# Kernel tuning notes

Hardware: AMD Instinct MI355X
Metric: run time of the kernel (lower is better)

## Reference

```python
import jax, jax.numpy as jnp
import numpy as np

SM_SCALE = 0.08838834764831845  # 1/sqrt(128)
SLIDING_WINDOW = 128
N_TOKENS, N_HEADS, Q_MULT, D_HEAD = 2048, 8, 4, 128


def setup_inputs() -> dict:
    key = jax.random.key(0)
    k1, k2, k3, k4 = jax.random.split(key, 4)
    Q = jax.random.normal(k1, (N_TOKENS, N_HEADS, Q_MULT, D_HEAD), dtype=jnp.float32)
    K = jax.random.normal(k2, (N_TOKENS, N_HEADS, D_HEAD), dtype=jnp.float32)
    V = jax.random.normal(k3, (N_TOKENS, N_HEADS, D_HEAD), dtype=jnp.float32)
    S = jax.random.normal(k4, (N_HEADS * Q_MULT,), dtype=jnp.float32)
    return {"Q": Q, "K": K, "V": V, "S": S}


def _build_mask(n_tokens, sliding_window, dtype):
    q_idx = jnp.arange(n_tokens)[:, None]
    k_idx = jnp.arange(n_tokens)[None, :]
    # causal: disallow k > q; sliding window: disallow k <= q - sliding_window
    disallowed = k_idx > q_idx
    if sliding_window > 0:
        disallowed = disallowed | (k_idx <= q_idx - sliding_window)
    return jnp.where(disallowed, jnp.array(-jnp.inf, dtype), jnp.array(0.0, dtype))


def reference(Q, K, V, S):
    n_tokens, n_heads, q_mult, d_head = Q.shape
    mask = _build_mask(n_tokens, SLIDING_WINDOW, Q.dtype)  # (T, T)
    # scores: (h, m, q, k)
    QK = jnp.einsum('qhmd,khd->hmqk', Q, K) * SM_SCALE
    QK = QK + mask[None, None, :, :]
    # append per-(head, q_mult) sink logit as an extra key column
    sink = jnp.broadcast_to(S.reshape(n_heads, q_mult, 1, 1),
                            (n_heads, q_mult, n_tokens, 1))
    QK = jnp.concatenate([QK, sink], axis=-1)  # (h, m, q, k+1)
    W = jax.nn.softmax(QK, axis=-1)[..., :-1]  # drop sink column
    attn = jnp.einsum('hmqk,khd->qhmd', W, V)
    return attn.reshape(n_tokens, n_heads * q_mult * d_head)
```

## Files before the change

kernel.cpp:

```cpp
#include <hip/hip_runtime.h>
#include <cstdint>

#define T_TOK 2048
#define NH 8
#define QM 4
#define DH 128
#define BQ 32
#define ROWS 128
#define CK 32
#define KS 136
#define VS 40
#define PS 40
#define SM_SCALE 0.08838834764831845f

typedef __attribute__((ext_vector_type(8))) short short8v;
typedef __attribute__((ext_vector_type(4))) short short4v;
typedef __attribute__((ext_vector_type(4))) float floatx4;

static __device__ __forceinline__ short f2bf(float x) {
  union { float f; unsigned u; } v; v.f = x;
  return (short)((v.u + 0x7fffu + ((v.u >> 16) & 1u)) >> 16);
}

__global__ __launch_bounds__(512, 4)
void attn_fwd(const float* __restrict__ Qp, const float* __restrict__ Kp,
              const float* __restrict__ Vp, const float* __restrict__ Sp,
              float* __restrict__ Op) {
  __shared__ short k_s[2][CK * KS];
  __shared__ short v_s[2][DH * VS];
  __shared__ short p_s[ROWS * PS];

  const int t    = threadIdx.x;
  const int lane = t & 63;
  const int wv   = t >> 6;
  const int quad = lane >> 4;
  const int l16  = lane & 15;

  const int bx = blockIdx.x;
  const int h  = bx & 7;
  const int q0 = (bx >> 3) * BQ;
  const int lo0 = q0 > 127 ? q0 - 127 : 0;
  const int nk  = q0 + BQ - lo0;
  const int nch = (nk + CK - 1) >> 5;

  const int Ra = wv * 16 + l16;
  const int qa = q0 + (Ra >> 2), ma = Ra & 3;
  const float* qptr = Qp + ((size_t)qa * (NH * QM) + h * QM + ma) * DH + quad * 8;
  short8v qf[4];
#pragma unroll
  for (int s = 0; s < 4; ++s) {
    float4 x0 = *(const float4*)(qptr + 32 * s);
    float4 x1 = *(const float4*)(qptr + 32 * s + 4);
    short8v f;
    f[0] = f2bf(x0.x); f[1] = f2bf(x0.y); f[2] = f2bf(x0.z); f[3] = f2bf(x0.w);
    f[4] = f2bf(x1.x); f[5] = f2bf(x1.y); f[6] = f2bf(x1.z); f[7] = f2bf(x1.w);
    qf[s] = f;
  }

  const int kj  = t >> 5;
  const int kd4 = (t & 31) * 4;
  const int vd  = t & 127;
  const int vg  = t >> 7;

  const int qc = q0 + wv * 4 + quad;
  float dn[4] = {0.f, 0.f, 0.f, 0.f};
  floatx4 oacc[8];
#pragma unroll
  for (int nt = 0; nt < 8; ++nt) oacc[nt] = (floatx4)0.0f;

  float4 pk[2];
  float  pv[8];
  {
    const int kb = lo0;
#pragma unroll
    for (int p = 0; p < 2; ++p) {
      int g = kb + kj + 16 * p; g = g < T_TOK ? g : T_TOK - 1;
      pk[p] = *(const float4*)(Kp + ((size_t)g * NH + h) * DH + kd4);
    }
#pragma unroll
    for (int j = 0; j < 8; ++j) {
      int g = kb + vg * 8 + j; g = g < T_TOK ? g : T_TOK - 1;
      pv[j] = Vp[((size_t)g * NH + h) * DH + vd];
    }
  }

  for (int c = 0; c < nch; ++c) {
    const int b  = c & 1;
    const int kb = lo0 + c * CK;

#pragma unroll
    for (int p = 0; p < 2; ++p) {
      short4v s4;
      s4[0] = f2bf(pk[p].x); s4[1] = f2bf(pk[p].y);
      s4[2] = f2bf(pk[p].z); s4[3] = f2bf(pk[p].w);
      *(short4v*)(&k_s[b][(kj + 16 * p) * KS + kd4]) = s4;
    }
    {
      short8v s8;
#pragma unroll
      for (int j = 0; j < 8; ++j) s8[j] = f2bf(pv[j]);
      *(short8v*)(&v_s[b][vd * VS + vg * 8]) = s8;
    }
    __syncthreads();

    if (c + 1 < nch) {
      const int kb2 = kb + CK;
#pragma unroll
      for (int p = 0; p < 2; ++p) {
        int g = kb2 + kj + 16 * p; g = g < T_TOK ? g : T_TOK - 1;
        pk[p] = *(const float4*)(Kp + ((size_t)g * NH + h) * DH + kd4);
      }
#pragma unroll
      for (int j = 0; j < 8; ++j) {
        int g = kb2 + vg * 8 + j; g = g < T_TOK ? g : T_TOK - 1;
        pv[j] = Vp[((size_t)g * NH + h) * DH + vd];
      }
    }

    floatx4 sc0 = (floatx4)0.0f, sc1 = (floatx4)0.0f;
#pragma unroll
    for (int s = 0; s < 4; ++s) {
      short8v k0 = *(const short8v*)(&k_s[b][l16 * KS + quad * 8 + 32 * s]);
      short8v k1 = *(const short8v*)(&k_s[b][(l16 + 16) * KS + quad * 8 + 32 * s]);
      sc0 = __builtin_amdgcn_mfma_f32_16x16x32_bf16(qf[s], k0, sc0, 0, 0, 0);
      sc1 = __builtin_amdgcn_mfma_f32_16x16x32_bf16(qf[s], k1, sc1, 0, 0, 0);
    }

    const int k0i = kb + l16, k1i = kb + 16 + l16;
    const bool ok0 = (k0i <= qc) && (k0i > qc - 128);
    const bool ok1 = (k1i <= qc) && (k1i > qc - 128);
#pragma unroll
    for (int r = 0; r < 4; ++r) {
      float e0 = ok0 ? __expf(sc0[r] * SM_SCALE) : 0.f;
      float e1 = ok1 ? __expf(sc1[r] * SM_SCALE) : 0.f;
      dn[r] += e0 + e1;
      const int R = wv * 16 + quad * 4 + r;
      p_s[R * PS + l16]      = f2bf(e0);
      p_s[R * PS + 16 + l16] = f2bf(e1);
    }

    short8v pf = *(const short8v*)(&p_s[(wv * 16 + l16) * PS + quad * 8]);
#pragma unroll
    for (int nt = 0; nt < 8; ++nt) {
      short8v vf = *(const short8v*)(&v_s[b][(l16 + 16 * nt) * VS + quad * 8]);
      oacc[nt] = __builtin_amdgcn_mfma_f32_16x16x32_bf16(pf, vf, oacc[nt], 0, 0, 0);
    }
  }

#pragma unroll
  for (int r = 0; r < 4; ++r) {
    float s = dn[r];
#pragma unroll
    for (int mm = 1; mm <= 8; mm <<= 1) s += __shfl_xor(s, mm);
    const float total = s + __expf(Sp[h * QM + r]);
    const float rd = 1.0f / total;
    float* ob = Op + (size_t)qc * (NH * QM * DH) + ((size_t)h * QM + r) * DH + l16;
#pragma unroll
    for (int nt = 0; nt < 8; ++nt) ob[nt * 16] = oacc[nt][r] * rd;
  }
}

extern "C" void kernel_launch(void* const* d_in, const int* in_sizes, int n_in,
                              void* d_out, int out_size, void* d_ws, size_t ws_size,
                              hipStream_t stream) {
  const float* Q = (const float*)d_in[0];
  const float* K = (const float*)d_in[1];
  const float* V = (const float*)d_in[2];
  const float* S = (const float*)d_in[3];
  float* O = (float*)d_out;
  const int grid = (T_TOK / BQ) * NH;
  attn_fwd<<<dim3(grid), dim3(512), 0, stream>>>(Q, K, V, S, O);
}
```

Baseline: 104.4 us.

## Double query tile per block and interleave keys for vectorized P stores

```diff
diff --git a/kernel.cpp b/kernel.cpp
--- a/kernel.cpp
+++ b/kernel.cpp
@@ -5,8 +5,8 @@
 #define NH 8
 #define QM 4
 #define DH 128
-#define BQ 32
-#define ROWS 128
+#define BQ 64
+#define ROWS 256
 #define CK 32
 #define KS 136
 #define VS 40
@@ -15,6 +15,7 @@
 
 typedef __attribute__((ext_vector_type(8))) short short8v;
 typedef __attribute__((ext_vector_type(4))) short short4v;
+typedef __attribute__((ext_vector_type(2))) short short2v;
 typedef __attribute__((ext_vector_type(4))) float floatx4;
 
 static __device__ __forceinline__ short f2bf(float x) {
@@ -22,7 +23,7 @@
   return (short)((v.u + 0x7fffu + ((v.u >> 16) & 1u)) >> 16);
 }
 
-__global__ __launch_bounds__(512, 4)
+__global__ __launch_bounds__(1024, 4)
 void attn_fwd(const float* __restrict__ Qp, const float* __restrict__ Kp,
               const float* __restrict__ Vp, const float* __restrict__ Sp,
               float* __restrict__ Op) {
@@ -68,19 +69,17 @@
 #pragma unroll
   for (int nt = 0; nt < 8; ++nt) oacc[nt] = (floatx4)0.0f;
 
-  float4 pk[2];
-  float  pv[8];
+  float4 pk;
+  float  pv[4];
   {
-    const int kb = lo0;
+    int g = lo0 + kj; g = g < T_TOK ? g : T_TOK - 1;
+    pk = *(const float4*)(Kp + ((size_t)g * NH + h) * DH + kd4);
 #pragma unroll
-    for (int p = 0; p < 2; ++p) {
-      int g = kb + kj + 16 * p; g = g < T_TOK ? g : T_TOK - 1;
-      pk[p] = *(const float4*)(Kp + ((size_t)g * NH + h) * DH + kd4);
-    }
-#pragma unroll
-    for (int j = 0; j < 8; ++j) {
-      int g = kb + vg * 8 + j; g = g < T_TOK ? g : T_TOK - 1;
-      pv[j] = Vp[((size_t)g * NH + h) * DH + vd];
+    for (int u = 0; u < 4; ++u) {
+      const int s = vg * 4 + u;
+      int gk = lo0 + (s >> 1) + ((s & 1) << 4);
+      gk = gk < T_TOK ? gk : T_TOK - 1;
+      pv[u] = Vp[((size_t)gk * NH + h) * DH + vd];
     }
   }
 
@@ -88,32 +87,26 @@
     const int b  = c & 1;
     const int kb = lo0 + c * CK;
 
-#pragma unroll
-    for (int p = 0; p < 2; ++p) {
+    {
       short4v s4;
-      s4[0] = f2bf(pk[p].x); s4[1] = f2bf(pk[p].y);
-      s4[2] = f2bf(pk[p].z); s4[3] = f2bf(pk[p].w);
-      *(short4v*)(&k_s[b][(kj + 16 * p) * KS + kd4]) = s4;
-    }
-    {
-      short8v s8;
-#pragma unroll
-      for (int j = 0; j < 8; ++j) s8[j] = f2bf(pv[j]);
-      *(short8v*)(&v_s[b][vd * VS + vg * 8]) = s8;
+      s4[0] = f2bf(pk.x); s4[1] = f2bf(pk.y); s4[2] = f2bf(pk.z); s4[3] = f2bf(pk.w);
+      *(short4v*)(&k_s[b][kj * KS + kd4]) = s4;
+      short4v t4;
+      t4[0] = f2bf(pv[0]); t4[1] = f2bf(pv[1]); t4[2] = f2bf(pv[2]); t4[3] = f2bf(pv[3]);
+      *(short4v*)(&v_s[b][vd * VS + vg * 4]) = t4;
     }
     __syncthreads();
 
     if (c + 1 < nch) {
       const int kb2 = kb + CK;
+      int g = kb2 + kj; g = g < T_TOK ? g : T_TOK - 1;
+      pk = *(const float4*)(Kp + ((size_t)g * NH + h) * DH + kd4);
 #pragma unroll
-      for (int p = 0; p < 2; ++p) {
-        int g = kb2 + kj + 16 * p; g = g < T_TOK ? g : T_TOK - 1;
-        pk[p] = *(const float4*)(Kp + ((size_t)g * NH + h) * DH + kd4);
-      }
-#pragma unroll
-      for (int j = 0; j < 8; ++j) {
-        int g = kb2 + vg * 8 + j; g = g < T_TOK ? g : T_TOK - 1;
-        pv[j] = Vp[((size_t)g * NH + h) * DH + vd];
+      for (int u = 0; u < 4; ++u) {
+        const int s = vg * 4 + u;
+        int gk = kb2 + (s >> 1) + ((s & 1) << 4);
+        gk = gk < T_TOK ? gk : T_TOK - 1;
+        pv[u] = Vp[((size_t)gk * NH + h) * DH + vd];
       }
     }
 
@@ -135,8 +128,8 @@
       float e1 = ok1 ? __expf(sc1[r] * SM_SCALE) : 0.f;
       dn[r] += e0 + e1;
       const int R = wv * 16 + quad * 4 + r;
-      p_s[R * PS + l16]      = f2bf(e0);
-      p_s[R * PS + 16 + l16] = f2bf(e1);
+      short2v p2; p2[0] = f2bf(e0); p2[1] = f2bf(e1);
+      *(short2v*)(&p_s[R * PS + 2 * l16]) = p2;
     }
 
     short8v pf = *(const short8v*)(&p_s[(wv * 16 + l16) * PS + quad * 8]);
@@ -169,5 +162,5 @@
   const float* S = (const float*)d_in[3];
   float* O = (float*)d_out;
   const int grid = (T_TOK / BQ) * NH;
-  attn_fwd<<<dim3(grid), dim3(512), 0, stream>>>(Q, K, V, S, O);
+  attn_fwd<<<dim3(grid), dim3(1024), 0, stream>>>(Q, K, V, S, O);
 }
```

Measured after the change: 103.9 us. Within noise of the previous version (-0.5%).
